# Optimization experiments

Measured on AMD Instinct MI355X. Metric: run time of the kernel, lower is better.

## Reference

```python
import jax, jax.numpy as jnp
import numpy as np

N_ROW = 50000
N_COL = 50000
E = 1_200_000
D_IN = 64
D_H = 128


def _gconv(h_src, src, dst, w_e, W, b, n_src, n_dst):
    """DGL GraphConv(norm='both') with edge weights: symmetric degree norm
    (unweighted degrees, clamped to >=1), u_mul_e message, sum reduce, then linear."""
    ones = jnp.ones_like(w_e)
    out_deg = jnp.clip(jax.ops.segment_sum(ones, src, num_segments=n_src), 1.0)
    in_deg = jnp.clip(jax.ops.segment_sum(ones, dst, num_segments=n_dst), 1.0)
    hs = h_src * jax.lax.rsqrt(out_deg)[:, None]          # [n_src, F] pre-norm
    m = hs[src] * w_e[:, None]                            # [E, F] gather + edge weight
    agg = jax.ops.segment_sum(m, dst, num_segments=n_dst)  # [n_dst, F] scatter-sum
    agg = agg * jax.lax.rsqrt(in_deg)[:, None]
    return agg @ W + b


def setup_inputs() -> dict:
    key = jax.random.key(0)
    ks = jax.random.split(key, 16)
    return {
        'feat_row': jax.random.normal(ks[0], (N_ROW, D_IN), jnp.float32),
        'feat_col': jax.random.normal(ks[1], (N_COL, D_IN), jnp.float32),
        'src_rc': jax.random.randint(ks[2], (E,), 0, N_ROW),
        'dst_rc': jax.random.randint(ks[3], (E,), 0, N_COL),
        'w_rc': jax.random.uniform(ks[4], (E,), jnp.float32),
        'src_cr': jax.random.randint(ks[5], (E,), 0, N_COL),
        'dst_cr': jax.random.randint(ks[6], (E,), 0, N_ROW),
        'w_cr': jax.random.uniform(ks[7], (E,), jnp.float32),
        'W0_rc': jax.random.normal(ks[8], (D_IN, D_H), jnp.float32) / np.float32(np.sqrt(D_IN)),
        'b0_rc': jnp.zeros((D_H,), jnp.float32),
        'W0_cr': jax.random.normal(ks[9], (D_IN, D_H), jnp.float32) / np.float32(np.sqrt(D_IN)),
        'b0_cr': jnp.zeros((D_H,), jnp.float32),
        'W1_rc': jax.random.normal(ks[10], (D_H, D_H), jnp.float32) / np.float32(np.sqrt(D_H)),
        'b1_rc': jnp.zeros((D_H,), jnp.float32),
        'W1_cr': jax.random.normal(ks[11], (D_H, D_H), jnp.float32) / np.float32(np.sqrt(D_H)),
        'b1_cr': jnp.zeros((D_H,), jnp.float32),
    }


def reference(feat_row, feat_col, src_rc, dst_rc, w_rc, src_cr, dst_cr, w_cr,
              W0_rc, b0_rc, W0_cr, b0_cr, W1_rc, b1_rc, W1_cr, b1_cr):
    # Layer 1 (HeteroGraphConv, sum across relations; each dst type has one relation) + ReLU
    h_col1 = jax.nn.relu(_gconv(feat_row, src_rc, dst_rc, w_rc, W0_rc, b0_rc, N_ROW, N_COL))
    h_row1 = jax.nn.relu(_gconv(feat_col, src_cr, dst_cr, w_cr, W0_cr, b0_cr, N_COL, N_ROW))
    # Layer 2 + ReLU
    h_col2 = jax.nn.relu(_gconv(h_row1, src_rc, dst_rc, w_rc, W1_rc, b1_rc, N_ROW, N_COL))
    h_row2 = jax.nn.relu(_gconv(h_col1, src_cr, dst_cr, w_cr, W1_cr, b1_cr, N_COL, N_ROW))
    # dgl.mean_nodes per ntype (single graph -> [1, D_H]), summed over ntypes
    hg = jnp.mean(h_row2, axis=0, keepdims=True) + jnp.mean(h_col2, axis=0, keepdims=True)
    return hg
```

## Files before the change

kernel.cpp:

```cpp
#include <hip/hip_runtime.h>

constexpr int NROW = 50000;
constexpr int NCOL = 50000;
constexpr int DH   = 128;
constexpr int NTAB = 200000;
constexpr int HB   = 12500;
constexpr int HBLK = 64;
constexpr int DGRID = 1250;
constexpr int GGRID = 2048;
constexpr int CH    = 500;

typedef __attribute__((ext_vector_type(8))) short short8;
typedef __attribute__((ext_vector_type(4))) float f32x4;

__device__ __forceinline__ float bf_lo(unsigned u) { return __uint_as_float(u << 16); }
__device__ __forceinline__ float bf_hi(unsigned u) { return __uint_as_float(u & 0xffff0000u); }
__device__ __forceinline__ unsigned short f2bf(float f) {
    unsigned u = __float_as_uint(f);
    return (unsigned short)((u + 0x7fffu + ((u >> 16) & 1u)) >> 16);
}

__global__ __launch_bounds__(512) void hist_lds(
        const int* __restrict__ s_rc, const int* __restrict__ d_rc,
        const int* __restrict__ s_cr, const int* __restrict__ d_cr,
        int* __restrict__ partial, int E) {
    __shared__ int h[HB];
    const int sec = blockIdx.x >> 6;
    const int blk = blockIdx.x & (HBLK - 1);
    const int tab = sec >> 2;
    const int lo  = (sec & 3) * HB;
    const int* __restrict__ arr = (tab == 0) ? s_rc : (tab == 1) ? d_rc
                                 : (tab == 2) ? s_cr : d_cr;
    for (int i = threadIdx.x; i < HB; i += blockDim.x) h[i] = 0;
    __syncthreads();
    const int stride = HBLK * blockDim.x;
    for (int i = blk * blockDim.x + threadIdx.x; i < E; i += stride) {
        int id = arr[i] - lo;
        if ((unsigned)id < (unsigned)HB) atomicAdd(&h[id], 1);
    }
    __syncthreads();
    int* __restrict__ out = partial + ((size_t)sec * HBLK + blk) * HB;
    for (int i = threadIdx.x; i < HB; i += blockDim.x) out[i] = h[i];
}

__global__ void reduce_norms2(const int* __restrict__ partial, int* __restrict__ cnt,
                              float* __restrict__ norms) {
    int stride = gridDim.x * blockDim.x;
    for (int i = blockIdx.x * blockDim.x + threadIdx.x; i < NTAB; i += stride) {
        int t = i / 50000;
        int r = i - t * 50000;
        int q = r / HB;
        int j = r - q * HB;
        const int* __restrict__ p = partial + ((size_t)(t * 4 + q) * HBLK) * HB + j;
        int s = 0;
#pragma unroll
        for (int b = 0; b < HBLK; ++b) s += p[(size_t)b * HB];
        cnt[i] = s;
        norms[i] = 1.0f / sqrtf((float)max(s, 1));
    }
}

__global__ __launch_bounds__(256) void scanA(const int* __restrict__ cnt, int* __restrict__ bsum) {
    __shared__ int red[256];
    const int c = blockIdx.x;
    const int* __restrict__ cbl = cnt + ((c >= 100) ? 150000 : 50000);
    const int j0 = (c % 100) * CH;
    int s = 0;
    for (int i = threadIdx.x; i < CH; i += 256) s += cbl[j0 + i];
    red[threadIdx.x] = s;
    __syncthreads();
    for (int off = 128; off > 0; off >>= 1) {
        if (threadIdx.x < off) red[threadIdx.x] += red[threadIdx.x + off];
        __syncthreads();
    }
    if (threadIdx.x == 0) bsum[c] = red[0];
}

__global__ void scanB(const int* __restrict__ bsum, int* __restrict__ cbase) {
    __shared__ int b[200];
    for (int i = threadIdx.x; i < 200; i += blockDim.x) b[i] = bsum[i];
    __syncthreads();
    if (threadIdx.x < 2) {
        int run = 0;
        const int o = threadIdx.x * 100;
        for (int k = 0; k < 100; ++k) { cbase[o + k] = run; run += b[o + k]; }
    }
}

__global__ __launch_bounds__(512) void scanC(const int* __restrict__ cnt,
                                             const int* __restrict__ cbase,
                                             int* __restrict__ ptr_rc, int* __restrict__ ptr_cr,
                                             int E) {
    __shared__ int buf[512];
    const int c = blockIdx.x;
    const int table = (c >= 100);
    const int* __restrict__ cbl = cnt + (table ? 150000 : 50000);
    int* __restrict__ ptr = table ? ptr_cr : ptr_rc;
    const int j0 = (c % 100) * CH;
    const int t = threadIdx.x;
    const int v = (t < CH) ? cbl[j0 + t] : 0;
    buf[t] = v;
    __syncthreads();
    for (int off = 1; off < 512; off <<= 1) {
        int tmp = (t >= off) ? buf[t - off] : 0;
        __syncthreads();
        buf[t] += tmp;
        __syncthreads();
    }
    if (t < CH) ptr[j0 + t] = cbase[c] + buf[t] - v;
    if ((c % 100) == 99 && t == 0) ptr[50000] = E;
}

__global__ void block_starts(int* __restrict__ partial,
                             const int* __restrict__ ptr_rc, const int* __restrict__ ptr_cr) {
    int stride = gridDim.x * blockDim.x;
    for (int i = blockIdx.x * blockDim.x + threadIdx.x; i < 8 * HB; i += stride) {
        int fsec = i / HB;
        int j = i - fsec * HB;
        int rel = fsec >> 2, q = fsec & 3;
        int histsec = rel * 8 + 4 + q;
        const int* __restrict__ ptr = rel ? ptr_cr : ptr_rc;
        int run = ptr[q * HB + j];
        int* __restrict__ p = partial + ((size_t)histsec * HBLK) * HB + j;
#pragma unroll
        for (int b = 0; b < HBLK; ++b) {
            int c = p[(size_t)b * HB];
            p[(size_t)b * HB] = run;
            run += c;
        }
    }
}

__global__ __launch_bounds__(512) void csr_fill_sorted(
        const int* __restrict__ sA, const int* __restrict__ dA,
        const float* __restrict__ wA, const float* __restrict__ routA, unsigned* __restrict__ pairA,
        const int* __restrict__ sB, const int* __restrict__ dB,
        const float* __restrict__ wB, const float* __restrict__ routB, unsigned* __restrict__ pairB,
        const int* __restrict__ partial, int E) {
    __shared__ int offs[HB];
    const int fsec = blockIdx.x >> 6;
    const int blk  = blockIdx.x & (HBLK - 1);
    const int rel = fsec >> 2, q = fsec & 3;
    const int histsec = rel * 8 + 4 + q;
    const int lo = q * HB;
    const int* __restrict__ src  = rel ? sB : sA;
    const int* __restrict__ dst  = rel ? dB : dA;
    const float* __restrict__ w  = rel ? wB : wA;
    const float* __restrict__ ro = rel ? routB : routA;
    unsigned* __restrict__ pair  = rel ? pairB : pairA;
    const int* __restrict__ bs = partial + ((size_t)histsec * HBLK + blk) * HB;
    for (int i = threadIdx.x; i < HB; i += blockDim.x) offs[i] = bs[i];
    __syncthreads();
    const int stride = HBLK * blockDim.x;
    for (int i = blk * blockDim.x + threadIdx.x; i < E; i += stride) {
        int id = dst[i] - lo;
        if ((unsigned)id < (unsigned)HB) {
            int pos = atomicAdd(&offs[id], 1);
            int s = src[i];
            pair[pos] = (unsigned)s | ((unsigned)f2bf(w[i] * ro[s]) << 16);
        }
    }
}

__global__ void prep_tables(const float4* __restrict__ fr, const float4* __restrict__ fc,
                            ushort4* __restrict__ br, ushort4* __restrict__ bc, int nq,
                            const float* __restrict__ W0a, const float* __restrict__ W0b,
                            const float* __restrict__ W1a, const float* __restrict__ W1b,
                            unsigned short* __restrict__ wt) {
    const int total = 2 * nq + 49152;
    int stride = gridDim.x * blockDim.x;
    for (int i = blockIdx.x * blockDim.x + threadIdx.x; i < total; i += stride) {
        if (i < 2 * nq) {
            bool second = i >= nq;
            int k = second ? i - nq : i;
            float4 v = second ? fc[k] : fr[k];
            ushort4 o;
            o.x = f2bf(v.x); o.y = f2bf(v.y); o.z = f2bf(v.z); o.w = f2bf(v.w);
            if (second) bc[k] = o; else br[k] = o;
        } else {
            int j = i - 2 * nq;
            const float* W; int K, base;
            if (j < 8192)       { W = W0a; K = 64;  base = 0; }
            else if (j < 16384) { W = W0b; K = 64;  base = 8192;  j -= 8192; }
            else if (j < 32768) { W = W1a; K = 128; base = 16384; j -= 16384; }
            else                { W = W1b; K = 128; base = 32768; j -= 32768; }
            int n = j / K, k = j - n * K;
            wt[base + n * K + k] = f2bf(W[k * DH + n]);
        }
    }
}

__global__ void gather64_2(const unsigned short* __restrict__ hA, const int* __restrict__ ptrA,
                           const unsigned* __restrict__ pairA, unsigned short* __restrict__ aggA,
                           const unsigned short* __restrict__ hB, const int* __restrict__ ptrB,
                           const unsigned* __restrict__ pairB, unsigned short* __restrict__ aggB,
                           int n) {
    const int rel  = blockIdx.x >= GGRID;
    const int bid  = rel ? blockIdx.x - GGRID : blockIdx.x;
    const unsigned short* __restrict__ h = rel ? hB : hA;
    const int* __restrict__ ptr  = rel ? ptrB : ptrA;
    const unsigned* __restrict__ pair = rel ? pairB : pairA;
    unsigned short* __restrict__ agg  = rel ? aggB : aggA;
    const int gw   = (bid * blockDim.x + threadIdx.x) >> 6;
    const int nw   = (GGRID * blockDim.x) >> 6;
    const int lane = threadIdx.x & 63;
    const int half = lane >> 5;
    const int c    = (lane & 31) << 1;
    for (int node = gw; node < n; node += nw) {
        const int beg = ptr[node], end = ptr[node + 1];
        float ax0 = 0.f, ay0 = 0.f, ax1 = 0.f, ay1 = 0.f;
        float ax2 = 0.f, ay2 = 0.f, ax3 = 0.f, ay3 = 0.f;
        int j = beg + half;
        for (; j + 6 < end; j += 8) {
            unsigned p0 = pair[j], p1 = pair[j + 2], p2 = pair[j + 4], p3 = pair[j + 6];
            unsigned h0 = *reinterpret_cast<const unsigned*>(&h[(size_t)(p0 & 0xffffu) * 64 + c]);
            unsigned h1 = *reinterpret_cast<const unsigned*>(&h[(size_t)(p1 & 0xffffu) * 64 + c]);
            unsigned h2 = *reinterpret_cast<const unsigned*>(&h[(size_t)(p2 & 0xffffu) * 64 + c]);
            unsigned h3 = *reinterpret_cast<const unsigned*>(&h[(size_t)(p3 & 0xffffu) * 64 + c]);
            float w0 = bf_hi(p0), w1 = bf_hi(p1), w2 = bf_hi(p2), w3 = bf_hi(p3);
            ax0 = fmaf(bf_lo(h0), w0, ax0); ay0 = fmaf(bf_hi(h0), w0, ay0);
            ax1 = fmaf(bf_lo(h1), w1, ax1); ay1 = fmaf(bf_hi(h1), w1, ay1);
            ax2 = fmaf(bf_lo(h2), w2, ax2); ay2 = fmaf(bf_hi(h2), w2, ay2);
            ax3 = fmaf(bf_lo(h3), w3, ax3); ay3 = fmaf(bf_hi(h3), w3, ay3);
        }
        for (; j < end; j += 2) {
            unsigned p = pair[j];
            unsigned hv = *reinterpret_cast<const unsigned*>(&h[(size_t)(p & 0xffffu) * 64 + c]);
            float w = bf_hi(p);
            ax0 = fmaf(bf_lo(hv), w, ax0); ay0 = fmaf(bf_hi(hv), w, ay0);
        }
        float ax = (ax0 + ax1) + (ax2 + ax3);
        float ay = (ay0 + ay1) + (ay2 + ay3);
        ax += __shfl_xor(ax, 32);
        ay += __shfl_xor(ay, 32);
        if (half == 0) {
            unsigned pk = (unsigned)f2bf(ax) | ((unsigned)f2bf(ay) << 16);
            *reinterpret_cast<unsigned*>(&agg[(size_t)node * 64 + c]) = pk;
        }
    }
}

__global__ void gather128_2(const unsigned short* __restrict__ hA, const int* __restrict__ ptrA,
                            const unsigned* __restrict__ pairA, unsigned short* __restrict__ aggA,
                            const unsigned short* __restrict__ hB, const int* __restrict__ ptrB,
                            const unsigned* __restrict__ pairB, unsigned short* __restrict__ aggB,
                            int n) {
    const int rel  = blockIdx.x >= GGRID;
    const int bid  = rel ? blockIdx.x - GGRID : blockIdx.x;
    const unsigned short* __restrict__ h = rel ? hB : hA;
    const int* __restrict__ ptr  = rel ? ptrB : ptrA;
    const unsigned* __restrict__ pair = rel ? pairB : pairA;
    unsigned short* __restrict__ agg  = rel ? aggB : aggA;
    const int gw   = (bid * blockDim.x + threadIdx.x) >> 6;
    const int nw   = (GGRID * blockDim.x) >> 6;
    const int lane = threadIdx.x & 63;
    const int c    = lane << 1;
    for (int node = gw; node < n; node += nw) {
        const int beg = ptr[node], end = ptr[node + 1];
        float ax[8], ay[8];
#pragma unroll
        for (int u = 0; u < 8; ++u) { ax[u] = 0.f; ay[u] = 0.f; }
        int j = beg;
        for (; j + 7 < end; j += 8) {
            unsigned p[8], hv[8];
#pragma unroll
            for (int u = 0; u < 8; ++u) p[u] = pair[j + u];
#pragma unroll
            for (int u = 0; u < 8; ++u)
                hv[u] = *reinterpret_cast<const unsigned*>(&h[(size_t)(p[u] & 0xffffu) * 128 + c]);
#pragma unroll
            for (int u = 0; u < 8; ++u) {
                float w = bf_hi(p[u]);
                ax[u] = fmaf(bf_lo(hv[u]), w, ax[u]);
                ay[u] = fmaf(bf_hi(hv[u]), w, ay[u]);
            }
        }
        for (; j < end; ++j) {
            unsigned p = pair[j];
            unsigned hv = *reinterpret_cast<const unsigned*>(&h[(size_t)(p & 0xffffu) * 128 + c]);
            float w = bf_hi(p);
            ax[0] = fmaf(bf_lo(hv), w, ax[0]); ay[0] = fmaf(bf_hi(hv), w, ay[0]);
        }
        float rx = ((ax[0] + ax[1]) + (ax[2] + ax[3])) + ((ax[4] + ax[5]) + (ax[6] + ax[7]));
        float ry = ((ay[0] + ay[1]) + (ay[2] + ay[3])) + ((ay[4] + ay[5]) + (ay[6] + ay[7]));
        unsigned pk = (unsigned)f2bf(rx) | ((unsigned)f2bf(ry) << 16);
        *reinterpret_cast<unsigned*>(&agg[(size_t)node * 128 + c]) = pk;
    }
}

template <int K, bool MEANSUM>
__global__ __launch_bounds__(256) void dense_mfma2(
        const unsigned short* __restrict__ aggA, const float* __restrict__ rinA,
        const unsigned short* __restrict__ wtA, const float* __restrict__ bA,
        unsigned short* __restrict__ outA, float* __restrict__ partA,
        const unsigned short* __restrict__ aggB, const float* __restrict__ rinB,
        const unsigned short* __restrict__ wtB, const float* __restrict__ bB,
        unsigned short* __restrict__ outB, float* __restrict__ partB,
        int n, float invn) {
    constexpr int NCH = K / 32;
    const int rel = blockIdx.x >= DGRID;
    const int bid = rel ? blockIdx.x - DGRID : blockIdx.x;
    const unsigned short* __restrict__ agg = rel ? aggB : aggA;
    const float* __restrict__ rin = rel ? rinB : rinA;
    const unsigned short* __restrict__ wt = rel ? wtB : wtA;
    const float* __restrict__ b = rel ? bB : bA;
    unsigned short* __restrict__ outbf = rel ? outB : outA;
    float* __restrict__ partial = rel ? partB : partA;

    const int wave = threadIdx.x >> 6;
    const int lane = threadIdx.x & 63;
    const int lrow = lane & 15;
    const int kgrp = lane >> 4;
    const int c0   = wave * 32;

    short8 bfr[2][NCH];
#pragma unroll
    for (int t = 0; t < 2; ++t)
#pragma unroll
        for (int ch = 0; ch < NCH; ++ch)
            bfr[t][ch] = *reinterpret_cast<const short8*>(
                &wt[(size_t)(c0 + t * 16 + lrow) * K + ch * 32 + kgrp * 8]);

    const float bias0 = b[c0 + lrow], bias1 = b[c0 + 16 + lrow];
    float acc0 = 0.f, acc1 = 0.f;

    const int nstrip = n >> 4;
    for (int s = bid; s < nstrip; s += DGRID) {
        const int r0 = s << 4;
        f32x4 d0 = {0.f, 0.f, 0.f, 0.f}, d1 = {0.f, 0.f, 0.f, 0.f};
#pragma unroll
        for (int ch = 0; ch < NCH; ++ch) {
            short8 af = *reinterpret_cast<const short8*>(
                &agg[(size_t)(r0 + lrow) * K + ch * 32 + kgrp * 8]);
            d0 = __builtin_amdgcn_mfma_f32_16x16x32_bf16(af, bfr[0][ch], d0, 0, 0, 0);
            d1 = __builtin_amdgcn_mfma_f32_16x16x32_bf16(af, bfr[1][ch], d1, 0, 0, 0);
        }
#pragma unroll
        for (int i = 0; i < 4; ++i) {
            const int row = r0 + kgrp * 4 + i;
            const float rv = rin[row];
            const float v0 = fmaxf(fmaf(rv, d0[i], bias0), 0.f);
            const float v1 = fmaxf(fmaf(rv, d1[i], bias1), 0.f);
            if (MEANSUM) { acc0 += v0; acc1 += v1; }
            else {
                outbf[(size_t)row * DH + c0 + lrow]      = f2bf(v0);
                outbf[(size_t)row * DH + c0 + 16 + lrow] = f2bf(v1);
            }
        }
    }
    if (MEANSUM) {
        acc0 += __shfl_xor(acc0, 16); acc0 += __shfl_xor(acc0, 32);
        acc1 += __shfl_xor(acc1, 16); acc1 += __shfl_xor(acc1, 32);
        if (kgrp == 0) {
            partial[(size_t)bid * DH + c0 + lrow]      = acc0 * invn;
            partial[(size_t)bid * DH + c0 + 16 + lrow] = acc1 * invn;
        }
    }
}

__global__ void reduce_out(const float* __restrict__ partial, float* __restrict__ out, int nrows) {
    const int t = threadIdx.x;
    const int per = nrows / gridDim.x;
    const int b0 = blockIdx.x * per;
    float s = 0.f;
    for (int b = b0; b < b0 + per; ++b) s += partial[(size_t)b * DH + t];
    atomicAdd(&out[t], s);
}

extern "C" void kernel_launch(void* const* d_in, const int* in_sizes, int n_in,
                              void* d_out, int out_size, void* d_ws, size_t ws_size,
                              hipStream_t stream) {
    const float* feat_row = (const float*)d_in[0];
    const float* feat_col = (const float*)d_in[1];
    const int*   src_rc   = (const int*)d_in[2];
    const int*   dst_rc   = (const int*)d_in[3];
    const float* w_rc     = (const float*)d_in[4];
    const int*   src_cr   = (const int*)d_in[5];
    const int*   dst_cr   = (const int*)d_in[6];
    const float* w_cr     = (const float*)d_in[7];
    const float* W0_rc    = (const float*)d_in[8];
    const float* b0_rc    = (const float*)d_in[9];
    const float* W0_cr    = (const float*)d_in[10];
    const float* b0_cr    = (const float*)d_in[11];
    const float* W1_rc    = (const float*)d_in[12];
    const float* b1_rc    = (const float*)d_in[13];
    const float* W1_cr    = (const float*)d_in[14];
    const float* b1_cr    = (const float*)d_in[15];
    const int E = in_sizes[2];
    float* out = (float*)d_out;

    int*   cnt     = (int*)d_ws;
    float* norms   = (float*)(cnt + 200000);
    int*   ptr_rc  = (int*)(norms + 200000);
    int*   ptr_cr  = ptr_rc + 50004;
    int*   bsum    = ptr_cr + 50004;
    int*   cbase   = bsum + 200;
    unsigned* pair_rc = (unsigned*)(cbase + 216);
    unsigned* pair_cr = pair_rc + E;
    unsigned short* agg_col = (unsigned short*)(pair_cr + E);
    unsigned short* agg_row = agg_col + (size_t)NCOL * DH;
    unsigned short* bf_row  = agg_row + (size_t)NROW * DH;
    unsigned short* bf_col  = bf_row + (size_t)NROW * 64;
    unsigned short* h_col1  = bf_col + (size_t)NCOL * 64;
    unsigned short* h_row1  = h_col1 + (size_t)NCOL * DH;
    float* partsum = (float*)(h_row1 + (size_t)NROW * DH);
    unsigned short* wt = (unsigned short*)(partsum + (size_t)2 * DGRID * DH);
    int* partial = (int*)agg_col;

    float* r_out_rc = norms;
    float* r_in_rc  = norms + NROW;
    float* r_out_cr = norms + NROW + NCOL;
    float* r_in_cr  = norms + NROW + 2 * NCOL;

    unsigned short* wt0_rc = wt;
    unsigned short* wt0_cr = wt + 8192;
    unsigned short* wt1_rc = wt + 16384;
    unsigned short* wt1_cr = wt + 32768;

    hist_lds<<<16 * HBLK, 512, 0, stream>>>(src_rc, dst_rc, src_cr, dst_cr, partial, E);
    reduce_norms2<<<512, 256, 0, stream>>>(partial, cnt, norms);
    scanA<<<200, 256, 0, stream>>>(cnt, bsum);
    scanB<<<1, 256, 0, stream>>>(bsum, cbase);
    scanC<<<200, 512, 0, stream>>>(cnt, cbase, ptr_rc, ptr_cr, E);
    block_starts<<<400, 256, 0, stream>>>(partial, ptr_rc, ptr_cr);
    csr_fill_sorted<<<8 * HBLK, 512, 0, stream>>>(
        src_rc, dst_rc, w_rc, r_out_rc, pair_rc,
        src_cr, dst_cr, w_cr, r_out_cr, pair_cr, partial, E);

    prep_tables<<<2048, 256, 0, stream>>>((const float4*)feat_row, (const float4*)feat_col,
                                          (ushort4*)bf_row, (ushort4*)bf_col, NROW * 64 / 4,
                                          W0_rc, W0_cr, W1_rc, W1_cr, wt);

    gather64_2<<<2 * GGRID, 256, 0, stream>>>(bf_row, ptr_rc, pair_rc, agg_col,
                                              bf_col, ptr_cr, pair_cr, agg_row, NCOL);
    dense_mfma2<64, false><<<2 * DGRID, 256, 0, stream>>>(
        agg_col, r_in_rc, wt0_rc, b0_rc, h_col1, nullptr,
        agg_row, r_in_cr, wt0_cr, b0_cr, h_row1, nullptr, NCOL, 0.f);

    hipMemsetAsync(out, 0, DH * sizeof(float), stream);

    gather128_2<<<2 * GGRID, 256, 0, stream>>>(h_row1, ptr_rc, pair_rc, agg_col,
                                               h_col1, ptr_cr, pair_cr, agg_row, NCOL);
    dense_mfma2<128, true><<<2 * DGRID, 256, 0, stream>>>(
        agg_col, r_in_rc, wt1_rc, b1_rc, nullptr, partsum,
        agg_row, r_in_cr, wt1_cr, b1_cr, nullptr, partsum + (size_t)DGRID * DH,
        NCOL, 1.0f / NCOL);
    reduce_out<<<50, 128, 0, stream>>>(partsum, out, 2 * DGRID);
}
```

Baseline: 355.3 us.

## Transform-then-aggregate in layer 2, store gathered features as FP8

Layer 2 is reordered so each source node's hidden state is multiplied by W1 first (new h1t_gemm2). The transformed rows are then gathered, and bias, ReLU and the mean are fused into the gather kernel, so the separate dense pass and its aggregate buffer round-trip are dropped. Both the layer-1 input features and the layer-2 transformed features are stored as FP8 e4m3, which halves the bytes each random gather reads. The cost is a large loss of precision that may break the tolerance, plus a software FP8 encoder on the write side.

```diff
diff --git a/kernel.cpp b/kernel.cpp
--- a/kernel.cpp
+++ b/kernel.cpp
@@ -1,4 +1,5 @@
 #include <hip/hip_runtime.h>
+#include <stdint.h>
 
 constexpr int NROW = 50000;
 constexpr int NCOL = 50000;
@@ -12,13 +13,45 @@
 
 typedef __attribute__((ext_vector_type(8))) short short8;
 typedef __attribute__((ext_vector_type(4))) float f32x4;
-
-__device__ __forceinline__ float bf_lo(unsigned u) { return __uint_as_float(u << 16); }
+typedef __attribute__((ext_vector_type(2))) float f32x2;
+
 __device__ __forceinline__ float bf_hi(unsigned u) { return __uint_as_float(u & 0xffff0000u); }
 __device__ __forceinline__ unsigned short f2bf(float f) {
     unsigned u = __float_as_uint(f);
     return (unsigned short)((u + 0x7fffu + ((u >> 16) & 1u)) >> 16);
 }
+
+__device__ __forceinline__ unsigned char f2fp8(float f) {
+    unsigned b = __float_as_uint(f);
+    unsigned s = (b >> 24) & 0x80u;
+    unsigned mag = b & 0x7fffffffu;
+    if (mag >= 0x43e00000u) return (unsigned char)(s | 0x7eu);
+    unsigned r = mag + 0x7ffffu + ((mag >> 20) & 1u);
+    int e = (int)(r >> 23) - 120;
+    if (e < 1) {
+        float af = __uint_as_float(mag);
+        unsigned m = (unsigned)(af * 512.f + 0.5f);
+        if (m > 8u) m = 8u;
+        return (unsigned char)(s | m);
+    }
+    return (unsigned char)(s | (unsigned)(e << 3) | ((r >> 20) & 7u));
+}
+
+#if defined(__has_builtin) && __has_builtin(__builtin_amdgcn_cvt_pk_f32_fp8)
+__device__ __forceinline__ f32x2 fp8x2f(unsigned v) {
+    return __builtin_amdgcn_cvt_pk_f32_fp8((int)v, false);
+}
+#else
+__device__ __forceinline__ float fp8_1(unsigned u) {
+    unsigned s = (u & 0x80u) << 24, em = u & 0x7fu;
+    if (em >= 8u) return __uint_as_float(s | ((em + 960u) << 20));
+    float v = (float)em * 0.001953125f;
+    return (u & 0x80u) ? -v : v;
+}
+__device__ __forceinline__ f32x2 fp8x2f(unsigned v) {
+    f32x2 r; r.x = fp8_1(v & 0xffu); r.y = fp8_1((v >> 8) & 0xffu); return r;
+}
+#endif
 
 __global__ __launch_bounds__(512) void hist_lds(
         const int* __restrict__ s_rc, const int* __restrict__ d_rc,
@@ -163,7 +196,7 @@
 }
 
 __global__ void prep_tables(const float4* __restrict__ fr, const float4* __restrict__ fc,
-                            ushort4* __restrict__ br, ushort4* __restrict__ bc, int nq,
+                            unsigned* __restrict__ f8r, unsigned* __restrict__ f8c, int nq,
                             const float* __restrict__ W0a, const float* __restrict__ W0b,
                             const float* __restrict__ W1a, const float* __restrict__ W1b,
                             unsigned short* __restrict__ wt) {
@@ -174,9 +207,9 @@
             bool second = i >= nq;
             int k = second ? i - nq : i;
             float4 v = second ? fc[k] : fr[k];
-            ushort4 o;
-            o.x = f2bf(v.x); o.y = f2bf(v.y); o.z = f2bf(v.z); o.w = f2bf(v.w);
-            if (second) bc[k] = o; else br[k] = o;
+            unsigned o = (unsigned)f2fp8(v.x) | ((unsigned)f2fp8(v.y) << 8)
+                       | ((unsigned)f2fp8(v.z) << 16) | ((unsigned)f2fp8(v.w) << 24);
+            if (second) f8c[k] = o; else f8r[k] = o;
         } else {
             int j = i - 2 * nq;
             const float* W; int K, base;
@@ -190,14 +223,14 @@
     }
 }
 
-__global__ void gather64_2(const unsigned short* __restrict__ hA, const int* __restrict__ ptrA,
+__global__ void gather64_2(const uint8_t* __restrict__ hA, const int* __restrict__ ptrA,
                            const unsigned* __restrict__ pairA, unsigned short* __restrict__ aggA,
-                           const unsigned short* __restrict__ hB, const int* __restrict__ ptrB,
+                           const uint8_t* __restrict__ hB, const int* __restrict__ ptrB,
                            const unsigned* __restrict__ pairB, unsigned short* __restrict__ aggB,
                            int n) {
     const int rel  = blockIdx.x >= GGRID;
     const int bid  = rel ? blockIdx.x - GGRID : blockIdx.x;
-    const unsigned short* __restrict__ h = rel ? hB : hA;
+    const uint8_t* __restrict__ h = rel ? hB : hA;
     const int* __restrict__ ptr  = rel ? ptrB : ptrA;
     const unsigned* __restrict__ pair = rel ? pairB : pairA;
     unsigned short* __restrict__ agg  = rel ? aggB : aggA;
@@ -213,21 +246,23 @@
         int j = beg + half;
         for (; j + 6 < end; j += 8) {
             unsigned p0 = pair[j], p1 = pair[j + 2], p2 = pair[j + 4], p3 = pair[j + 6];
-            unsigned h0 = *reinterpret_cast<const unsigned*>(&h[(size_t)(p0 & 0xffffu) * 64 + c]);
-            unsigned h1 = *reinterpret_cast<const unsigned*>(&h[(size_t)(p1 & 0xffffu) * 64 + c]);
-            unsigned h2 = *reinterpret_cast<const unsigned*>(&h[(size_t)(p2 & 0xffffu) * 64 + c]);
-            unsigned h3 = *reinterpret_cast<const unsigned*>(&h[(size_t)(p3 & 0xffffu) * 64 + c]);
+            unsigned h0 = *reinterpret_cast<const unsigned short*>(&h[(size_t)(p0 & 0xffffu) * 64 + c]);
+            unsigned h1 = *reinterpret_cast<const unsigned short*>(&h[(size_t)(p1 & 0xffffu) * 64 + c]);
+            unsigned h2 = *reinterpret_cast<const unsigned short*>(&h[(size_t)(p2 & 0xffffu) * 64 + c]);
+            unsigned h3 = *reinterpret_cast<const unsigned short*>(&h[(size_t)(p3 & 0xffffu) * 64 + c]);
+            f32x2 d0 = fp8x2f(h0), d1 = fp8x2f(h1), d2 = fp8x2f(h2), d3 = fp8x2f(h3);
             float w0 = bf_hi(p0), w1 = bf_hi(p1), w2 = bf_hi(p2), w3 = bf_hi(p3);
-            ax0 = fmaf(bf_lo(h0), w0, ax0); ay0 = fmaf(bf_hi(h0), w0, ay0);
-            ax1 = fmaf(bf_lo(h1), w1, ax1); ay1 = fmaf(bf_hi(h1), w1, ay1);
-            ax2 = fmaf(bf_lo(h2), w2, ax2); ay2 = fmaf(bf_hi(h2), w2, ay2);
-            ax3 = fmaf(bf_lo(h3), w3, ax3); ay3 = fmaf(bf_hi(h3), w3, ay3);
+            ax0 = fmaf(d0.x, w0, ax0); ay0 = fmaf(d0.y, w0, ay0);
+            ax1 = fmaf(d1.x, w1, ax1); ay1 = fmaf(d1.y, w1, ay1);
+            ax2 = fmaf(d2.x, w2, ax2); ay2 = fmaf(d2.y, w2, ay2);
+            ax3 = fmaf(d3.x, w3, ax3); ay3 = fmaf(d3.y, w3, ay3);
         }
         for (; j < end; j += 2) {
             unsigned p = pair[j];
-            unsigned hv = *reinterpret_cast<const unsigned*>(&h[(size_t)(p & 0xffffu) * 64 + c]);
+            unsigned hv = *reinterpret_cast<const unsigned short*>(&h[(size_t)(p & 0xffffu) * 64 + c]);
+            f32x2 d = fp8x2f(hv);
             float w = bf_hi(p);
-            ax0 = fmaf(bf_lo(hv), w, ax0); ay0 = fmaf(bf_hi(hv), w, ay0);
+            ax0 = fmaf(d.x, w, ax0); ay0 = fmaf(d.y, w, ay0);
         }
         float ax = (ax0 + ax1) + (ax2 + ax3);
         float ay = (ay0 + ay1) + (ay2 + ay3);
@@ -240,64 +275,14 @@
     }
 }
 
-__global__ void gather128_2(const unsigned short* __restrict__ hA, const int* __restrict__ ptrA,
-                            const unsigned* __restrict__ pairA, unsigned short* __restrict__ aggA,
-                            const unsigned short* __restrict__ hB, const int* __restrict__ ptrB,
-                            const unsigned* __restrict__ pairB, unsigned short* __restrict__ aggB,
-                            int n) {
-    const int rel  = blockIdx.x >= GGRID;
-    const int bid  = rel ? blockIdx.x - GGRID : blockIdx.x;
-    const unsigned short* __restrict__ h = rel ? hB : hA;
-    const int* __restrict__ ptr  = rel ? ptrB : ptrA;
-    const unsigned* __restrict__ pair = rel ? pairB : pairA;
-    unsigned short* __restrict__ agg  = rel ? aggB : aggA;
-    const int gw   = (bid * blockDim.x + threadIdx.x) >> 6;
-    const int nw   = (GGRID * blockDim.x) >> 6;
-    const int lane = threadIdx.x & 63;
-    const int c    = lane << 1;
-    for (int node = gw; node < n; node += nw) {
-        const int beg = ptr[node], end = ptr[node + 1];
-        float ax[8], ay[8];
-#pragma unroll
-        for (int u = 0; u < 8; ++u) { ax[u] = 0.f; ay[u] = 0.f; }
-        int j = beg;
-        for (; j + 7 < end; j += 8) {
-            unsigned p[8], hv[8];
-#pragma unroll
-            for (int u = 0; u < 8; ++u) p[u] = pair[j + u];
-#pragma unroll
-            for (int u = 0; u < 8; ++u)
-                hv[u] = *reinterpret_cast<const unsigned*>(&h[(size_t)(p[u] & 0xffffu) * 128 + c]);
-#pragma unroll
-            for (int u = 0; u < 8; ++u) {
-                float w = bf_hi(p[u]);
-                ax[u] = fmaf(bf_lo(hv[u]), w, ax[u]);
-                ay[u] = fmaf(bf_hi(hv[u]), w, ay[u]);
-            }
-        }
-        for (; j < end; ++j) {
-            unsigned p = pair[j];
-            unsigned hv = *reinterpret_cast<const unsigned*>(&h[(size_t)(p & 0xffffu) * 128 + c]);
-            float w = bf_hi(p);
-            ax[0] = fmaf(bf_lo(hv), w, ax[0]); ay[0] = fmaf(bf_hi(hv), w, ay[0]);
-        }
-        float rx = ((ax[0] + ax[1]) + (ax[2] + ax[3])) + ((ax[4] + ax[5]) + (ax[6] + ax[7]));
-        float ry = ((ay[0] + ay[1]) + (ay[2] + ay[3])) + ((ay[4] + ay[5]) + (ay[6] + ay[7]));
-        unsigned pk = (unsigned)f2bf(rx) | ((unsigned)f2bf(ry) << 16);
-        *reinterpret_cast<unsigned*>(&agg[(size_t)node * 128 + c]) = pk;
-    }
-}
-
-template <int K, bool MEANSUM>
-__global__ __launch_bounds__(256) void dense_mfma2(
+__global__ __launch_bounds__(256) void dense64_2(
         const unsigned short* __restrict__ aggA, const float* __restrict__ rinA,
         const unsigned short* __restrict__ wtA, const float* __restrict__ bA,
-        unsigned short* __restrict__ outA, float* __restrict__ partA,
+        unsigned short* __restrict__ outA,
         const unsigned short* __restrict__ aggB, const float* __restrict__ rinB,
         const unsigned short* __restrict__ wtB, const float* __restrict__ bB,
-        unsigned short* __restrict__ outB, float* __restrict__ partB,
-        int n, float invn) {
-    constexpr int NCH = K / 32;
+        unsigned short* __restrict__ outB, int n) {
+    constexpr int K = 64, NCH = 2;
     const int rel = blockIdx.x >= DGRID;
     const int bid = rel ? blockIdx.x - DGRID : blockIdx.x;
     const unsigned short* __restrict__ agg = rel ? aggB : aggA;
@@ -305,7 +290,6 @@
     const unsigned short* __restrict__ wt = rel ? wtB : wtA;
     const float* __restrict__ b = rel ? bB : bA;
     unsigned short* __restrict__ outbf = rel ? outB : outA;
-    float* __restrict__ partial = rel ? partB : partA;
 
     const int wave = threadIdx.x >> 6;
     const int lane = threadIdx.x & 63;
@@ -322,8 +306,6 @@
                 &wt[(size_t)(c0 + t * 16 + lrow) * K + ch * 32 + kgrp * 8]);
 
     const float bias0 = b[c0 + lrow], bias1 = b[c0 + 16 + lrow];
-    float acc0 = 0.f, acc1 = 0.f;
-
     const int nstrip = n >> 4;
     for (int s = bid; s < nstrip; s += DGRID) {
         const int r0 = s << 4;
@@ -339,22 +321,127 @@
         for (int i = 0; i < 4; ++i) {
             const int row = r0 + kgrp * 4 + i;
             const float rv = rin[row];
-            const float v0 = fmaxf(fmaf(rv, d0[i], bias0), 0.f);
-            const float v1 = fmaxf(fmaf(rv, d1[i], bias1), 0.f);
-            if (MEANSUM) { acc0 += v0; acc1 += v1; }
-            else {
-                outbf[(size_t)row * DH + c0 + lrow]      = f2bf(v0);
-                outbf[(size_t)row * DH + c0 + 16 + lrow] = f2bf(v1);
+            outbf[(size_t)row * DH + c0 + lrow]      = f2bf(fmaxf(fmaf(rv, d0[i], bias0), 0.f));
+            outbf[(size_t)row * DH + c0 + 16 + lrow] = f2bf(fmaxf(fmaf(rv, d1[i], bias1), 0.f));
+        }
+    }
+}
+
+__global__ __launch_bounds__(256) void h1t_gemm2(
+        const unsigned short* __restrict__ hA, const unsigned short* __restrict__ wtA,
+        uint8_t* __restrict__ htA,
+        const unsigned short* __restrict__ hB, const unsigned short* __restrict__ wtB,
+        uint8_t* __restrict__ htB, int n) {
+    constexpr int K = 128, NCH = 4;
+    const int rel = blockIdx.x >= DGRID;
+    const int bid = rel ? blockIdx.x - DGRID : blockIdx.x;
+    const unsigned short* __restrict__ h = rel ? hB : hA;
+    const unsigned short* __restrict__ wt = rel ? wtB : wtA;
+    uint8_t* __restrict__ ht = rel ? htB : htA;
+
+    const int wave = threadIdx.x >> 6;
+    const int lane = threadIdx.x & 63;
+    const int lrow = lane & 15;
+    const int kgrp = lane >> 4;
+    const int c0   = wave * 32;
+
+    short8 bfr[2][NCH];
+#pragma unroll
+    for (int t = 0; t < 2; ++t)
+#pragma unroll
+        for (int ch = 0; ch < NCH; ++ch)
+            bfr[t][ch] = *reinterpret_cast<const short8*>(
+                &wt[(size_t)(c0 + t * 16 + lrow) * K + ch * 32 + kgrp * 8]);
+
+    const int nstrip = n >> 4;
+    for (int s = bid; s < nstrip; s += DGRID) {
+        const int r0 = s << 4;
+        f32x4 d0 = {0.f, 0.f, 0.f, 0.f}, d1 = {0.f, 0.f, 0.f, 0.f};
+#pragma unroll
+        for (int ch = 0; ch < NCH; ++ch) {
+            short8 af = *reinterpret_cast<const short8*>(
+                &h[(size_t)(r0 + lrow) * K + ch * 32 + kgrp * 8]);
+            d0 = __builtin_amdgcn_mfma_f32_16x16x32_bf16(af, bfr[0][ch], d0, 0, 0, 0);
+            d1 = __builtin_amdgcn_mfma_f32_16x16x32_bf16(af, bfr[1][ch], d1, 0, 0, 0);
+        }
+#pragma unroll
+        for (int i = 0; i < 4; ++i) {
+            const int row = r0 + kgrp * 4 + i;
+            ht[(size_t)row * DH + c0 + lrow]      = f2fp8(d0[i]);
+            ht[(size_t)row * DH + c0 + 16 + lrow] = f2fp8(d1[i]);
+        }
+    }
+}
+
+__global__ __launch_bounds__(256) void gather_final(
+        const uint8_t* __restrict__ htA, const int* __restrict__ ptrA,
+        const unsigned* __restrict__ pairA, const float* __restrict__ rinA,
+        const float* __restrict__ bA,
+        const uint8_t* __restrict__ htB, const int* __restrict__ ptrB,
+        const unsigned* __restrict__ pairB, const float* __restrict__ rinB,
+        const float* __restrict__ bB,
+        float* __restrict__ partsum, int n, float invn) {
+    const int rel  = blockIdx.x >= GGRID;
+    const int bid  = rel ? blockIdx.x - GGRID : blockIdx.x;
+    const uint8_t* __restrict__ ht = rel ? htB : htA;
+    const int* __restrict__ ptr  = rel ? ptrB : ptrA;
+    const unsigned* __restrict__ pair = rel ? pairB : pairA;
+    const float* __restrict__ rin = rel ? rinB : rinA;
+    const float* __restrict__ b   = rel ? bB : bA;
+
+    const int gw   = (bid * blockDim.x + threadIdx.x) >> 6;
+    const int nw   = (GGRID * blockDim.x) >> 6;
+    const int lane = threadIdx.x & 63;
+    const int c    = lane << 1;
+    const float bias0 = b[c], bias1 = b[c + 1];
+    float m0 = 0.f, m1 = 0.f;
+
+    for (int node = gw; node < n; node += nw) {
+        const int beg = ptr[node], end = ptr[node + 1];
+        float ax[8], ay[8];
+#pragma unroll
+        for (int u = 0; u < 8; ++u) { ax[u] = 0.f; ay[u] = 0.f; }
+        int j = beg;
+        for (; j + 7 < end; j += 8) {
+            unsigned p[8]; unsigned hv[8];
+#pragma unroll
+            for (int u = 0; u < 8; ++u) p[u] = pair[j + u];
+#pragma unroll
+            for (int u = 0; u < 8; ++u)
+                hv[u] = *reinterpret_cast<const unsigned short*>(&ht[(size_t)(p[u] & 0xffffu) * 128 + c]);
+#pragma unroll
+            for (int u = 0; u < 8; ++u) {
+                f32x2 d = fp8x2f(hv[u]);
+                float w = bf_hi(p[u]);
+                ax[u] = fmaf(d.x, w, ax[u]);
+                ay[u] = fmaf(d.y, w, ay[u]);
             }
         }
-    }
-    if (MEANSUM) {
-        acc0 += __shfl_xor(acc0, 16); acc0 += __shfl_xor(acc0, 32);
-        acc1 += __shfl_xor(acc1, 16); acc1 += __shfl_xor(acc1, 32);
-        if (kgrp == 0) {
-            partial[(size_t)bid * DH + c0 + lrow]      = acc0 * invn;
-            partial[(size_t)bid * DH + c0 + 16 + lrow] = acc1 * invn;
-        }
+        for (; j < end; ++j) {
+            unsigned p = pair[j];
+            unsigned hv = *reinterpret_cast<const unsigned short*>(&ht[(size_t)(p & 0xffffu) * 128 + c]);
+            f32x2 d = fp8x2f(hv);
+            float w = bf_hi(p);
+            ax[0] = fmaf(d.x, w, ax[0]); ay[0] = fmaf(d.y, w, ay[0]);
+        }
+        float accx = ((ax[0] + ax[1]) + (ax[2] + ax[3])) + ((ax[4] + ax[5]) + (ax[6] + ax[7]));
+        float accy = ((ay[0] + ay[1]) + (ay[2] + ay[3])) + ((ay[4] + ay[5]) + (ay[6] + ay[7]));
+        const float rv = rin[node];
+        m0 += fmaxf(fmaf(rv, accx, bias0), 0.f);
+        m1 += fmaxf(fmaf(rv, accy, bias1), 0.f);
+    }
+
+    __shared__ float red[512];
+    red[threadIdx.x] = m0;
+    red[256 + threadIdx.x] = m1;
+    __syncthreads();
+    if (threadIdx.x < 64) {
+        float s0 = red[threadIdx.x] + red[threadIdx.x + 64] + red[threadIdx.x + 128] + red[threadIdx.x + 192];
+        float s1 = red[256 + threadIdx.x] + red[256 + threadIdx.x + 64]
+                 + red[256 + threadIdx.x + 128] + red[256 + threadIdx.x + 192];
+        float* part = partsum + (size_t)blockIdx.x * DH;
+        part[2 * threadIdx.x]     = s0 * invn;
+        part[2 * threadIdx.x + 1] = s1 * invn;
     }
 }
 
@@ -398,13 +485,15 @@
     unsigned* pair_rc = (unsigned*)(cbase + 216);
     unsigned* pair_cr = pair_rc + E;
     unsigned short* agg_col = (unsigned short*)(pair_cr + E);
-    unsigned short* agg_row = agg_col + (size_t)NCOL * DH;
-    unsigned short* bf_row  = agg_row + (size_t)NROW * DH;
-    unsigned short* bf_col  = bf_row + (size_t)NROW * 64;
-    unsigned short* h_col1  = bf_col + (size_t)NCOL * 64;
-    unsigned short* h_row1  = h_col1 + (size_t)NCOL * DH;
-    float* partsum = (float*)(h_row1 + (size_t)NROW * DH);
-    unsigned short* wt = (unsigned short*)(partsum + (size_t)2 * DGRID * DH);
+    unsigned short* agg_row = agg_col + (size_t)NCOL * 64;
+    uint8_t* f8_row = (uint8_t*)(agg_row + (size_t)NROW * 64);
+    uint8_t* f8_col = f8_row + (size_t)NROW * 64;
+    unsigned short* h_col1 = (unsigned short*)(f8_col + (size_t)NCOL * 64);
+    unsigned short* h_row1 = h_col1 + (size_t)NCOL * DH;
+    uint8_t* ht_row = (uint8_t*)(h_row1 + (size_t)NROW * DH);
+    uint8_t* ht_col = ht_row + (size_t)NROW * DH;
+    float* partsum = (float*)(ht_col + (size_t)NCOL * DH);
+    unsigned short* wt = (unsigned short*)(partsum + (size_t)2 * GGRID * DH);
     int* partial = (int*)agg_col;
 
     float* r_out_rc = norms;
@@ -428,22 +517,20 @@
         src_cr, dst_cr, w_cr, r_out_cr, pair_cr, partial, E);
 
     prep_tables<<<2048, 256, 0, stream>>>((const float4*)feat_row, (const float4*)feat_col,
-                                          (ushort4*)bf_row, (ushort4*)bf_col, NROW * 64 / 4,
+                                          (unsigned*)f8_row, (unsigned*)f8_col, NROW * 64 / 4,
                                           W0_rc, W0_cr, W1_rc, W1_cr, wt);
 
-    gather64_2<<<2 * GGRID, 256, 0, stream>>>(bf_row, ptr_rc, pair_rc, agg_col,
-                                              bf_col, ptr_cr, pair_cr, agg_row, NCOL);
-    dense_mfma2<64, false><<<2 * DGRID, 256, 0, stream>>>(
-        agg_col, r_in_rc, wt0_rc, b0_rc, h_col1, nullptr,
-        agg_row, r_in_cr, wt0_cr, b0_cr, h_row1, nullptr, NCOL, 0.f);
-
+    gather64_2<<<2 * GGRID, 256, 0, stream>>>(f8_row, ptr_rc, pair_rc, agg_col,
+                                              f8_col, ptr_cr, pair_cr, agg_row, NCOL);
+    dense64_2<<<2 * DGRID, 256, 0, stream>>>(agg_col, r_in_rc, wt0_rc, b0_rc, h_col1,
+                                             agg_row, r_in_cr, wt0_cr, b0_cr, h_row1, NCOL);
+
+    h1t_gemm2<<<2 * DGRID, 256, 0, stream>>>(h_row1, wt1_rc, ht_row,
+                                             h_col1, wt1_cr, ht_col, NROW);
     hipMemsetAsync(out, 0, DH * sizeof(float), stream);
-
-    gather128_2<<<2 * GGRID, 256, 0, stream>>>(h_row1, ptr_rc, pair_rc, agg_col,
-                                               h_col1, ptr_cr, pair_cr, agg_row, NCOL);
-    dense_mfma2<128, true><<<2 * DGRID, 256, 0, stream>>>(
-        agg_col, r_in_rc, wt1_rc, b1_rc, nullptr, partsum,
-        agg_row, r_in_cr, wt1_cr, b1_cr, nullptr, partsum + (size_t)DGRID * DH,
-        NCOL, 1.0f / NCOL);
-    reduce_out<<<50, 128, 0, stream>>>(partsum, out, 2 * DGRID);
-}
+    gather_final<<<2 * GGRID, 256, 0, stream>>>(
+        ht_row, ptr_rc, pair_rc, r_in_rc, b1_rc,
+        ht_col, ptr_cr, pair_cr, r_in_cr, b1_cr,
+        partsum, NCOL, 1.0f / NCOL);
+    reduce_out<<<32, 128, 0, stream>>>(partsum, out, 2 * GGRID);
+}
```

New measurement: 335.4 us. 5.6% less time.
